# Optimization experiments

Hardware: AMD Instinct MI355X
Metric: run time of the kernel (lower is better)

## Reference

```python
import jax, jax.numpy as jnp
import numpy as np

SEQ, BATCH, HID = 4096, 32, 512


def setup_inputs() -> dict:
    key = jax.random.key(0)
    ks = jax.random.split(key, 7)
    s = 1.0 / np.sqrt(HID)
    return {
        "x0": jax.random.normal(ks[0], (SEQ, BATCH, 1), dtype=jnp.float32),
        "W_ih": jax.random.uniform(ks[1], (4 * HID, 1), jnp.float32, -s, s),
        "W_hh": jax.random.uniform(ks[2], (4 * HID, HID), jnp.float32, -s, s),
        "b_ih": jax.random.uniform(ks[3], (4 * HID,), jnp.float32, -s, s),
        "b_hh": jax.random.uniform(ks[4], (4 * HID,), jnp.float32, -s, s),
        "W_lin": jax.random.uniform(ks[5], (1, HID), jnp.float32, -s, s),
        "b_lin": jax.random.uniform(ks[6], (1,), jnp.float32, -s, s),
    }


def _lstm(x0, W_ih, W_hh, b_ih, b_hh):
    # x0: (T, B, 1). Precompute input contribution to gates for all steps.
    x_proj = jnp.einsum("tbi,gi->tbg", x0, W_ih) + (b_ih + b_hh)  # (T, B, 4H)
    T, B, _ = x_proj.shape
    H = W_hh.shape[1]
    h0 = jnp.zeros((B, H), x0.dtype)
    c0 = jnp.zeros((B, H), x0.dtype)

    def step(carry, xp):
        h, c = carry
        gates = xp + h @ W_hh.T  # (B, 4H)
        i, f, g, o = jnp.split(gates, 4, axis=-1)  # torch gate order i,f,g,o
        i = jax.nn.sigmoid(i)
        f = jax.nn.sigmoid(f)
        g = jnp.tanh(g)
        o = jax.nn.sigmoid(o)
        c = f * c + i * g
        h = o * jnp.tanh(c)
        return (h, c), h

    _, hs = jax.lax.scan(step, (h0, c0), x_proj)  # hs: (T, B, H)
    return hs


def reference(x0, W_ih, W_hh, b_ih, b_hh, W_lin, b_lin):
    hs = _lstm(x0, W_ih, W_hh, b_ih, b_hh)            # (T, B, H)
    y = jnp.einsum("tbh,oh->tbo", hs, W_lin) + b_lin  # (T, B, 1)
    return y + x0                                      # residual add
```

## Files before the change

### kernel.cpp

```cpp
#include <hip/hip_runtime.h>
#include <stdint.h>

#define T_STEPS 4096
#define BATCH 32
#define HID 512
#define GROUPS 8
#define BLK_THREADS 1024
#define NBLOCKS 256

typedef _Float16 h2_t __attribute__((ext_vector_type(2)));
typedef uint32_t u32x16 __attribute__((ext_vector_type(16)));

__device__ inline uint32_t pack_h2(float a, float b) {
  h2_t v;
  v.x = (_Float16)a;
  v.y = (_Float16)b;
  return __builtin_bit_cast(uint32_t, v);
}

__device__ inline float fdot2(uint32_t a, uint32_t b, float c) {
  return __builtin_amdgcn_fdot2(__builtin_bit_cast(h2_t, a),
                                __builtin_bit_cast(h2_t, b), c, false);
}

__device__ inline uint32_t aread(uint32_t a) {
  uint32_t v;
  asm("v_accvgpr_read_b32 %0, %1" : "=v"(v) : "a"(a));
  return v;
}

__device__ inline uint64_t uni64(const void* p) {
  uint32_t lo = __builtin_amdgcn_readfirstlane((uint32_t)(uintptr_t)p);
  uint32_t hi = __builtin_amdgcn_readfirstlane((uint32_t)((uintptr_t)p >> 32));
  return ((uint64_t)hi << 32) | lo;
}

__device__ inline void kinv() {
  asm volatile("s_dcache_inv" ::: "memory");
}
__device__ inline void sload64(uint64_t p, u32x16& h0, u32x16& h1,
                               u32x16& h2, u32x16& h3) {
  asm volatile(
      "s_load_dwordx16 %0, %4, 0x0\n\t"
      "s_load_dwordx16 %1, %4, 0x40\n\t"
      "s_load_dwordx16 %2, %4, 0x80\n\t"
      "s_load_dwordx16 %3, %4, 0xc0\n\t"
      "s_waitcnt lgkmcnt(0)"
      : "=s"(h0), "=s"(h1), "=s"(h2), "=s"(h3)
      : "s"(p) : "memory");
}

__device__ inline float sigf(float x) { return 1.0f / (1.0f + __expf(-x)); }
__device__ inline float tanh_fast(float x) {
  float a = fabsf(x);
  float e = __expf(-2.0f * a);
  float r = (1.0f - e) / (1.0f + e);
  return copysignf(r, x);
}

__global__ __launch_bounds__(BLK_THREADS)
void lstm_tag(const float* __restrict__ x0,
              const float* __restrict__ W_ih,
              const float* __restrict__ W_hh,
              const float* __restrict__ b_ih,
              const float* __restrict__ b_hh,
              const float* __restrict__ W_lin,
              const float* __restrict__ b_lin,
              float* __restrict__ y,
              uint32_t* __restrict__ h_ex,
              int* __restrict__ claim)
{
  __shared__ float x0_lds[T_STEPS];
  __shared__ float ylds[T_STEPS];
  __shared__ float gacc[2][256];
  __shared__ int s_bg;

  const int tid = threadIdx.x;

  if (tid == 0) {
    uint32_t xcc;
    asm volatile("s_getreg_b32 %0, hwreg(HW_REG_XCC_ID)" : "=s"(xcc));
    xcc &= 7;
    int slot = atomicAdd(claim + xcc * 16, 1);
    s_bg = (slot < 32) ? (int)(((4 * xcc + (slot >> 3)) << 3) | (slot & 7))
                       : -1;
  }
  __syncthreads();
  if (s_bg < 0) return;
  const int b  = s_bg >> 3;
  const int g  = s_bg & 7;
  const int u0 = g * 64;
  const int wv = tid >> 6;
  const int rg = wv >> 3;
  const int cs = wv & 7;
  const int l  = tid & 63;

  uint32_t a0[32], a1[32];
  {
    const int r0 = 128 * rg + l;
    const int r1 = r0 + 64;
    const int R0 = (r0 >> 6) * HID + u0 + (r0 & 63);
    const int R1 = (r1 >> 6) * HID + u0 + (r1 & 63);
    const float2* p0 = (const float2*)(W_hh + (size_t)R0 * HID + 64 * cs);
    const float2* p1 = (const float2*)(W_hh + (size_t)R1 * HID + 64 * cs);
#pragma unroll
    for (int k = 0; k < 32; ++k) {
      float2 a = p0[k], c = p1[k];
      uint32_t t0 = pack_h2(a.x, a.y);
      uint32_t t1 = pack_h2(c.x, c.y);
      asm("v_accvgpr_write_b32 %0, %1" : "=a"(a0[k]) : "v"(t0));
      asm("v_accvgpr_write_b32 %0, %1" : "=a"(a1[k]) : "v"(t1));
    }
  }
  for (int i = tid; i < T_STEPS; i += BLK_THREADS) {
    x0_lds[i] = x0[i * BATCH + b];
    ylds[i] = 0.f;
  }
  if (tid < 256) { gacc[0][tid] = 0.f; gacc[1][tid] = 0.f; }

  float c_state = 0.f;
  float wih_[4] = {0.f, 0.f, 0.f, 0.f}, bs_[4] = {0.f, 0.f, 0.f, 0.f};
  float wlin_u = 0.f, blin = 0.f;
  if (tid < 64) {
#pragma unroll
    for (int j = 0; j < 4; ++j) {
      int R = j * HID + u0 + tid;
      wih_[j] = W_ih[R];
      bs_[j] = b_ih[R] + b_hh[R];
    }
    wlin_u = W_lin[u0 + tid];
    blin = b_lin[0];
  }

  uint32_t* hb = h_ex + (size_t)b * 512;
  const uint64_t dpu[2] = { uni64(hb + 64 * cs),
                            uni64(hb + BATCH * 512 + 64 * cs) };
  uint32_t* pub01[2] = { hb + u0 + tid, hb + BATCH * 512 + u0 + tid };

  __syncthreads();

  int dead = 0;
  for (int t = 0; t < T_STEPS; ++t) {
    const int sl = t & 1, ns = sl ^ 1;

    u32x16 h0, h1, h2, h3;
    {
      const uint32_t tw = (uint32_t)t << 16;
      int guard = 0;
      for (;;) {
        kinv();
        sload64(dpu[sl], h0, h1, h2, h3);
        uint32_t bad = 0;
#pragma unroll
        for (int k = 0; k < 16; ++k) {
          bad |= (h0[k] ^ tw) | (h1[k] ^ tw) | (h2[k] ^ tw) | (h3[k] ^ tw);
        }
        if ((bad & 0xffff0000u) == 0u) break;
        if (dead || ++guard > (1 << 20)) { dead = 1; break; }
        __builtin_amdgcn_s_sleep(1);
      }
    }
    uint32_t pk[32];
#pragma unroll
    for (int e = 0; e < 8; ++e) {
      pk[e]      = (h0[2 * e] & 0xffffu) | (h0[2 * e + 1] << 16);
      pk[8 + e]  = (h1[2 * e] & 0xffffu) | (h1[2 * e + 1] << 16);
      pk[16 + e] = (h2[2 * e] & 0xffffu) | (h2[2 * e + 1] << 16);
      pk[24 + e] = (h3[2 * e] & 0xffffu) | (h3[2 * e + 1] << 16);
    }
    float acc0 = 0.f, acc1 = 0.f;
#pragma unroll
    for (int k = 0; k < 32; ++k) {
      acc0 = fdot2(aread(a0[k]), pk[k], acc0);
      acc1 = fdot2(aread(a1[k]), pk[k], acc1);
    }
    atomicAdd(&gacc[sl][128 * rg + l], acc0);
    atomicAdd(&gacc[sl][128 * rg + 64 + l], acc1);
    __syncthreads();

    if (tid < 64) {
      const float xv = x0_lds[t];
      float gi = gacc[sl][tid]       + xv * wih_[0] + bs_[0];
      float gf = gacc[sl][tid + 64]  + xv * wih_[1] + bs_[1];
      float gg = gacc[sl][tid + 128] + xv * wih_[2] + bs_[2];
      float go = gacc[sl][tid + 192] + xv * wih_[3] + bs_[3];
      float si = sigf(gi), sf = sigf(gf), tg_ = tanh_fast(gg), so = sigf(go);
      c_state = sf * c_state + si * tg_;
      float h = so * tanh_fast(c_state);

      uint16_t hbb = __builtin_bit_cast(uint16_t, (_Float16)h);
      pub01[ns][0] = ((uint32_t)(t + 1) << 16) | (uint32_t)hbb;

      gacc[sl][tid] = 0.f;
      gacc[sl][tid + 64] = 0.f;
      gacc[sl][tid + 128] = 0.f;
      gacc[sl][tid + 192] = 0.f;

      float p = wlin_u * h;
#pragma unroll
      for (int m = 32; m >= 1; m >>= 1) p += __shfl_xor(p, m, 64);
      if (tid == 0) ylds[t] = p;
    }
  }

  __syncthreads();
  for (int i = tid; i < T_STEPS; i += BLK_THREADS) {
    float val = ylds[i];
    if (g == 0) val += blin + x0_lds[i];
    unsafeAtomicAdd(&y[i * BATCH + b], val);
  }
}

extern "C" void kernel_launch(void* const* d_in, const int* in_sizes, int n_in,
                              void* d_out, int out_size, void* d_ws, size_t ws_size,
                              hipStream_t stream) {
  const float* x0    = (const float*)d_in[0];
  const float* W_ih  = (const float*)d_in[1];
  const float* W_hh  = (const float*)d_in[2];
  const float* b_ih  = (const float*)d_in[3];
  const float* b_hh  = (const float*)d_in[4];
  const float* W_lin = (const float*)d_in[5];
  const float* b_lin = (const float*)d_in[6];
  float* y = (float*)d_out;

  uint32_t* h_ex = (uint32_t*)d_ws;
  int* claim = (int*)(h_ex + 2 * BATCH * 512);
  const size_t init_bytes =
      (size_t)2 * BATCH * 512 * sizeof(uint32_t) + 8 * 16 * sizeof(int);

  (void)hipMemsetAsync(d_ws, 0, init_bytes, stream);
  (void)hipMemsetAsync(d_out, 0, (size_t)out_size * sizeof(float), stream);

  hipLaunchKernelGGL(lstm_tag, dim3(NBLOCKS), dim3(BLK_THREADS), 0, stream,
                     x0, W_ih, W_hh, b_ih, b_hh, W_lin, b_lin, y, h_ex, claim);
}
```

Measured before the change: 16.04 ms.

## Quantize recurrent weights and hidden state to int8 and halve blocks per batch

Replaces the fp16 fdot2 recurrent matvec with int8 sdot4, using per-row scales for W_hh and a fixed 127 scale for h. Each batch now uses 4 blocks of 128 hidden units instead of 8 of 64, so fewer blocks take part in the per-step cross-block h exchange. Two int8 h values are packed per tagged word and the LDS float atomics are replaced by per-slice int partial sums. This lowers precision considerably, since h quantized to 127 levels may drift over 4096 recurrent steps and break tolerance.

```diff
diff --git a/kernel.cpp b/kernel.cpp
--- a/kernel.cpp
+++ b/kernel.cpp
@@ -4,25 +4,27 @@
 #define T_STEPS 4096
 #define BATCH 32
 #define HID 512
-#define GROUPS 8
+#define GROUPS 4
 #define BLK_THREADS 1024
 #define NBLOCKS 256
 
-typedef _Float16 h2_t __attribute__((ext_vector_type(2)));
 typedef uint32_t u32x16 __attribute__((ext_vector_type(16)));
 
-__device__ inline uint32_t pack_h2(float a, float b) {
-  h2_t v;
-  v.x = (_Float16)a;
-  v.y = (_Float16)b;
-  return __builtin_bit_cast(uint32_t, v);
-}
-
-__device__ inline float fdot2(uint32_t a, uint32_t b, float c) {
-  return __builtin_amdgcn_fdot2(__builtin_bit_cast(h2_t, a),
-                                __builtin_bit_cast(h2_t, b), c, false);
-}
-
+__device__ inline int sdot4(uint32_t a, uint32_t b, int c) {
+#if __has_builtin(__builtin_amdgcn_sdot4)
+  return __builtin_amdgcn_sdot4((int)a, (int)b, c, false);
+#else
+  int d;
+  asm("v_dot4_i32_i8 %0, %1, %2, %3" : "=v"(d) : "v"(a), "v"(b), "v"(c));
+  return d;
+#endif
+}
+
+__device__ inline uint32_t awrite(uint32_t v) {
+  uint32_t a;
+  asm("v_accvgpr_write_b32 %0, %1" : "=a"(a) : "v"(v));
+  return a;
+}
 __device__ inline uint32_t aread(uint32_t a) {
   uint32_t v;
   asm("v_accvgpr_read_b32 %0, %1" : "=v"(v) : "a"(a));
@@ -34,7 +36,6 @@
   uint32_t hi = __builtin_amdgcn_readfirstlane((uint32_t)((uintptr_t)p >> 32));
   return ((uint64_t)hi << 32) | lo;
 }
-
 __device__ inline void kinv() {
   asm volatile("s_dcache_inv" ::: "memory");
 }
@@ -59,20 +60,21 @@
 }
 
 __global__ __launch_bounds__(BLK_THREADS)
-void lstm_tag(const float* __restrict__ x0,
-              const float* __restrict__ W_ih,
-              const float* __restrict__ W_hh,
-              const float* __restrict__ b_ih,
-              const float* __restrict__ b_hh,
-              const float* __restrict__ W_lin,
-              const float* __restrict__ b_lin,
-              float* __restrict__ y,
-              uint32_t* __restrict__ h_ex,
-              int* __restrict__ claim)
+void lstm_i8(const float* __restrict__ x0,
+             const float* __restrict__ W_ih,
+             const float* __restrict__ W_hh,
+             const float* __restrict__ b_ih,
+             const float* __restrict__ b_hh,
+             const float* __restrict__ W_lin,
+             const float* __restrict__ b_lin,
+             float* __restrict__ y,
+             uint32_t* __restrict__ h_ex,
+             int* __restrict__ claim)
 {
   __shared__ float x0_lds[T_STEPS];
   __shared__ float ylds[T_STEPS];
-  __shared__ float gacc[2][256];
+  __shared__ int   gacc[2][GROUPS][512];
+  __shared__ float rmax[512];
   __shared__ int s_bg;
 
   const int tid = threadIdx.x;
@@ -82,61 +84,94 @@
     asm volatile("s_getreg_b32 %0, hwreg(HW_REG_XCC_ID)" : "=s"(xcc));
     xcc &= 7;
     int slot = atomicAdd(claim + xcc * 16, 1);
-    s_bg = (slot < 32) ? (int)(((4 * xcc + (slot >> 3)) << 3) | (slot & 7))
+    s_bg = (slot < 16) ? (int)(((4 * xcc + (slot >> 2)) << 2) | (slot & 3))
                        : -1;
   }
   __syncthreads();
   if (s_bg < 0) return;
-  const int b  = s_bg >> 3;
-  const int g  = s_bg & 7;
-  const int u0 = g * 64;
+  const int b  = s_bg >> 2;
+  const int g  = s_bg & 3;
+  const int u0 = g * 128;
   const int wv = tid >> 6;
-  const int rg = wv >> 3;
-  const int cs = wv & 7;
+  const int rg = wv >> 2;
+  const int cs = wv & 3;
   const int l  = tid & 63;
 
-  uint32_t a0[32], a1[32];
-  {
-    const int r0 = 128 * rg + l;
-    const int r1 = r0 + 64;
-    const int R0 = (r0 >> 6) * HID + u0 + (r0 & 63);
-    const int R1 = (r1 >> 6) * HID + u0 + (r1 & 63);
-    const float2* p0 = (const float2*)(W_hh + (size_t)R0 * HID + 64 * cs);
-    const float2* p1 = (const float2*)(W_hh + (size_t)R1 * HID + 64 * cs);
-#pragma unroll
-    for (int k = 0; k < 32; ++k) {
-      float2 a = p0[k], c = p1[k];
-      uint32_t t0 = pack_h2(a.x, a.y);
-      uint32_t t1 = pack_h2(c.x, c.y);
-      asm("v_accvgpr_write_b32 %0, %1" : "=a"(a0[k]) : "v"(t0));
-      asm("v_accvgpr_write_b32 %0, %1" : "=a"(a1[k]) : "v"(t1));
-    }
-  }
   for (int i = tid; i < T_STEPS; i += BLK_THREADS) {
     x0_lds[i] = x0[i * BATCH + b];
     ylds[i] = 0.f;
   }
-  if (tid < 256) { gacc[0][tid] = 0.f; gacc[1][tid] = 0.f; }
-
+  if (tid < 512) rmax[tid] = 0.f;
+  {
+    int* gz = &gacc[0][0][0];
+    for (int i = tid; i < 2 * GROUPS * 512; i += BLK_THREADS) gz[i] = 0;
+  }
+  __syncthreads();
+
+  const int r0 = rg * 128 + l;
+  const int r1 = r0 + 64;
+  const int R0 = rg * HID + u0 + l;
+  const int R1 = R0 + 64;
+  const float4* p0 = (const float4*)(W_hh + (size_t)R0 * HID + 128 * cs);
+  const float4* p1 = (const float4*)(W_hh + (size_t)R1 * HID + 128 * cs);
+  {
+    float m0 = 1e-20f, m1 = 1e-20f;
+#pragma unroll
+    for (int k = 0; k < 32; ++k) {
+      float4 a = p0[k];
+      m0 = fmaxf(m0, fmaxf(fmaxf(fabsf(a.x), fabsf(a.y)),
+                           fmaxf(fabsf(a.z), fabsf(a.w))));
+      float4 c = p1[k];
+      m1 = fmaxf(m1, fmaxf(fmaxf(fabsf(c.x), fabsf(c.y)),
+                           fmaxf(fabsf(c.z), fabsf(c.w))));
+    }
+    atomicMax((int*)&rmax[r0], __float_as_int(m0));
+    atomicMax((int*)&rmax[r1], __float_as_int(m1));
+  }
+  __syncthreads();
+
+  uint32_t wa[64];
+  {
+    const float i0 = 127.0f / rmax[r0];
+    const float i1 = 127.0f / rmax[r1];
+#pragma unroll
+    for (int k = 0; k < 32; ++k) {
+      float4 a = p0[k];
+      int q0 = (int)rintf(a.x * i0), q1 = (int)rintf(a.y * i0);
+      int q2 = (int)rintf(a.z * i0), q3 = (int)rintf(a.w * i0);
+      wa[k] = awrite((uint32_t)((q0 & 0xff) | ((q1 & 0xff) << 8) |
+                                ((q2 & 0xff) << 16) | ((q3 & 0xff) << 24)));
+      float4 c = p1[k];
+      int s0 = (int)rintf(c.x * i1), s1 = (int)rintf(c.y * i1);
+      int s2 = (int)rintf(c.z * i1), s3 = (int)rintf(c.w * i1);
+      wa[32 + k] = awrite((uint32_t)((s0 & 0xff) | ((s1 & 0xff) << 8) |
+                                     ((s2 & 0xff) << 16) | ((s3 & 0xff) << 24)));
+    }
+  }
+
+  const int lu = wv * 8 + l;
+  const int U  = u0 + lu;
   float c_state = 0.f;
   float wih_[4] = {0.f, 0.f, 0.f, 0.f}, bs_[4] = {0.f, 0.f, 0.f, 0.f};
-  float wlin_u = 0.f, blin = 0.f;
-  if (tid < 64) {
+  float s_[4] = {0.f, 0.f, 0.f, 0.f};
+  float wlin_u = 0.f;
+  if (l < 8) {
 #pragma unroll
     for (int j = 0; j < 4; ++j) {
-      int R = j * HID + u0 + tid;
+      int R = j * HID + U;
       wih_[j] = W_ih[R];
       bs_[j] = b_ih[R] + b_hh[R];
-    }
-    wlin_u = W_lin[u0 + tid];
-    blin = b_lin[0];
-  }
-
-  uint32_t* hb = h_ex + (size_t)b * 512;
+      s_[j] = rmax[j * 128 + lu] * (1.0f / 16129.0f);
+    }
+    wlin_u = W_lin[U];
+  }
+  const float blin = b_lin[0];
+
+  uint32_t* hb = h_ex + (size_t)b * 256;
   const uint64_t dpu[2] = { uni64(hb + 64 * cs),
-                            uni64(hb + BATCH * 512 + 64 * cs) };
-  uint32_t* pub01[2] = { hb + u0 + tid, hb + BATCH * 512 + u0 + tid };
-
+                            uni64(hb + BATCH * 256 + 64 * cs) };
+  uint32_t* pubbase[2] = { hb + g * 64 + wv * 4,
+                           hb + BATCH * 256 + g * 64 + wv * 4 };
   __syncthreads();
 
   int dead = 0;
@@ -168,38 +203,46 @@
       pk[16 + e] = (h2[2 * e] & 0xffffu) | (h2[2 * e + 1] << 16);
       pk[24 + e] = (h3[2 * e] & 0xffffu) | (h3[2 * e + 1] << 16);
     }
-    float acc0 = 0.f, acc1 = 0.f;
+    int acc0 = 0, acc1 = 0;
 #pragma unroll
     for (int k = 0; k < 32; ++k) {
-      acc0 = fdot2(aread(a0[k]), pk[k], acc0);
-      acc1 = fdot2(aread(a1[k]), pk[k], acc1);
-    }
-    atomicAdd(&gacc[sl][128 * rg + l], acc0);
-    atomicAdd(&gacc[sl][128 * rg + 64 + l], acc1);
+      acc0 = sdot4(aread(wa[k]), pk[k], acc0);
+      acc1 = sdot4(aread(wa[32 + k]), pk[k], acc1);
+    }
+    gacc[sl][cs][r0] = acc0;
+    gacc[sl][cs][r1] = acc1;
     __syncthreads();
 
-    if (tid < 64) {
+    if (l < 8) {
       const float xv = x0_lds[t];
-      float gi = gacc[sl][tid]       + xv * wih_[0] + bs_[0];
-      float gf = gacc[sl][tid + 64]  + xv * wih_[1] + bs_[1];
-      float gg = gacc[sl][tid + 128] + xv * wih_[2] + bs_[2];
-      float go = gacc[sl][tid + 192] + xv * wih_[3] + bs_[3];
-      float si = sigf(gi), sf = sigf(gf), tg_ = tanh_fast(gg), so = sigf(go);
-      c_state = sf * c_state + si * tg_;
+      float gi = (float)(gacc[sl][0][lu] + gacc[sl][1][lu] +
+                         gacc[sl][2][lu] + gacc[sl][3][lu]) * s_[0]
+                 + xv * wih_[0] + bs_[0];
+      float gf = (float)(gacc[sl][0][128 + lu] + gacc[sl][1][128 + lu] +
+                         gacc[sl][2][128 + lu] + gacc[sl][3][128 + lu]) * s_[1]
+                 + xv * wih_[1] + bs_[1];
+      float gg = (float)(gacc[sl][0][256 + lu] + gacc[sl][1][256 + lu] +
+                         gacc[sl][2][256 + lu] + gacc[sl][3][256 + lu]) * s_[2]
+                 + xv * wih_[2] + bs_[2];
+      float go = (float)(gacc[sl][0][384 + lu] + gacc[sl][1][384 + lu] +
+                         gacc[sl][2][384 + lu] + gacc[sl][3][384 + lu]) * s_[3]
+                 + xv * wih_[3] + bs_[3];
+      float si = sigf(gi), sf = sigf(gf), tg = tanh_fast(gg), so = sigf(go);
+      c_state = sf * c_state + si * tg;
       float h = so * tanh_fast(c_state);
 
-      uint16_t hbb = __builtin_bit_cast(uint16_t, (_Float16)h);
-      pub01[ns][0] = ((uint32_t)(t + 1) << 16) | (uint32_t)hbb;
-
-      gacc[sl][tid] = 0.f;
-      gacc[sl][tid + 64] = 0.f;
-      gacc[sl][tid + 128] = 0.f;
-      gacc[sl][tid + 192] = 0.f;
-
+      int q = (int)rintf(h * 127.0f);
+      int qn = __shfl_down(q, 1, 64);
+      if ((l & 1) == 0) {
+        pubbase[ns][l >> 1] = ((uint32_t)(t + 1) << 16) |
+                              ((uint32_t)(qn & 0xff) << 8) |
+                              (uint32_t)(q & 0xff);
+      }
       float p = wlin_u * h;
-#pragma unroll
-      for (int m = 32; m >= 1; m >>= 1) p += __shfl_xor(p, m, 64);
-      if (tid == 0) ylds[t] = p;
+      p += __shfl_xor(p, 1, 64);
+      p += __shfl_xor(p, 2, 64);
+      p += __shfl_xor(p, 4, 64);
+      if (l == 0) atomicAdd(&ylds[t], p);
     }
   }
 
@@ -224,13 +267,13 @@
   float* y = (float*)d_out;
 
   uint32_t* h_ex = (uint32_t*)d_ws;
-  int* claim = (int*)(h_ex + 2 * BATCH * 512);
+  int* claim = (int*)(h_ex + 2 * BATCH * 256);
   const size_t init_bytes =
-      (size_t)2 * BATCH * 512 * sizeof(uint32_t) + 8 * 16 * sizeof(int);
+      (size_t)2 * BATCH * 256 * sizeof(uint32_t) + 8 * 16 * sizeof(int);
 
   (void)hipMemsetAsync(d_ws, 0, init_bytes, stream);
   (void)hipMemsetAsync(d_out, 0, (size_t)out_size * sizeof(float), stream);
 
-  hipLaunchKernelGGL(lstm_tag, dim3(NBLOCKS), dim3(BLK_THREADS), 0, stream,
+  hipLaunchKernelGGL(lstm_i8, dim3(NBLOCKS), dim3(BLK_THREADS), 0, stream,
                      x0, W_ih, W_hh, b_ih, b_hh, W_lin, b_lin, y, h_ex, claim);
 }
```

Result: slower. 16.59 ms (+3.4%).
